# Kernel tuning notes

Measured on AMD Instinct MI355X. Metric: run time of the kernel, lower is better.

Reference implementation:

```python
import jax, jax.numpy as jnp
import numpy as np

TEMPERATURE = 0.07
EPS = 1e-8  # torch F.cosine_similarity eps


def reference(features):
    B, F, D = features.shape
    x = features.reshape(B * F, D)  # [N, D]
    # cosine similarity = normalized-dot; torch clamps norm at eps
    norm = jnp.maximum(jnp.linalg.norm(x, axis=-1, keepdims=True), EPS)
    xn = x / norm
    logits = (xn @ xn.T) / TEMPERATURE  # [N, N]
    # cross_entropy with labels = arange(N): mean(logsumexp - diagonal)
    lse = jax.scipy.special.logsumexp(logits, axis=-1)
    diag = jnp.diagonal(logits)
    return jnp.mean(lse - diag)


def setup_inputs() -> dict:
    key = jax.random.key(0)
    features = jax.random.normal(key, (512, 16, 512), dtype=jnp.float32)
    return {"features": features}
```

## Files before the change

### kernel.cpp

```cpp
#include <hip/hip_runtime.h>
#include <hip/hip_bf16.h>
#include <cstdint>

#define N_TOT 8192
#define DDIM  512
#define NBLK  64
#define NTRI  (NBLK * (NBLK + 1) / 2)
constexpr float INV_T = 1.0f / 0.07f;

typedef unsigned short u16;
typedef __attribute__((ext_vector_type(8))) short bf16x8_t;
typedef __attribute__((ext_vector_type(4))) float f32x4_t;


__device__ __forceinline__ u16 f2bf(float f) {
  uint32_t u = __float_as_uint(f);
  uint32_t r = (u + 0x7FFFu + ((u >> 16) & 1u)) >> 16;
  return (u16)r;
}

__device__ __forceinline__ void load16_to_lds(const void* g, void* l) {
  __builtin_amdgcn_global_load_lds(
      (const __attribute__((address_space(1))) unsigned int*)g,
      (__attribute__((address_space(3))) unsigned int*)l, 16, 0, 0);
}

__global__ __launch_bounds__(256) void normalize_kernel(const float* __restrict__ X,
                                                        u16* __restrict__ Xn,
                                                        float* __restrict__ tsum,
                                                        float* __restrict__ out) {
  if (blockIdx.x < 32) tsum[blockIdx.x * 256 + threadIdx.x] = 0.0f;
  if (blockIdx.x == 32 && threadIdx.x == 0) out[0] = 0.0f;
  const int lane = threadIdx.x & 63;
  const int row  = blockIdx.x * 4 + (threadIdx.x >> 6);
  const float4* xr = (const float4*)(X + (size_t)row * DDIM);
  float4 v0 = xr[lane];
  float4 v1 = xr[lane + 64];
  float s = v0.x * v0.x + v0.y * v0.y + v0.z * v0.z + v0.w * v0.w
          + v1.x * v1.x + v1.y * v1.y + v1.z * v1.z + v1.w * v1.w;
#pragma unroll
  for (int m = 1; m < 64; m <<= 1) s += __shfl_xor(s, m);
  const float scale = 1.0f / fmaxf(sqrtf(s), 1e-8f);
  ushort4 o0, o1;
  o0.x = f2bf(v0.x * scale); o0.y = f2bf(v0.y * scale);
  o0.z = f2bf(v0.z * scale); o0.w = f2bf(v0.w * scale);
  o1.x = f2bf(v1.x * scale); o1.y = f2bf(v1.y * scale);
  o1.z = f2bf(v1.z * scale); o1.w = f2bf(v1.w * scale);
  ushort4* orow = (ushort4*)(Xn + (size_t)row * DDIM);
  orow[lane]      = o0;
  orow[lane + 64] = o1;
}

__global__ __launch_bounds__(256, 4) void gemm_exp_rowsum(const u16* __restrict__ Xn,
                                                          float* __restrict__ tsum) {
  __shared__ __align__(16) u16 sA[128 * 64];
  __shared__ __align__(16) u16 sB[128 * 64];

  const int k = blockIdx.x;
  int bi = (int)((sqrtf(8.0f * (float)k + 1.0f) - 1.0f) * 0.5f);
  while ((bi + 1) * (bi + 2) / 2 <= k) ++bi;
  while (bi * (bi + 1) / 2 > k) --bi;
  const int bj = k - bi * (bi + 1) / 2;
  const int rowBase = bi * 128;
  const int colBase = bj * 128;
  const bool isDiag = (bi == bj);

  const int t    = threadIdx.x;
  const int lane = t & 63;
  const int l15  = lane & 15;
  const int quad = lane >> 4;
  const int w    = t >> 6;
  const int wm   = w >> 1;
  const int wn   = w & 1;

  f32x4_t acc[4][4];
#pragma unroll
  for (int i = 0; i < 4; i++)
#pragma unroll
    for (int j = 0; j < 4; j++) acc[i][j] = {0.f, 0.f, 0.f, 0.f};

  const int srow = t >> 3;
  const int jlog = ((t & 7) ^ (srow & 7)) * 8;
  const u16* gA = Xn + (size_t)(rowBase + srow) * DDIM + jlog;
  const u16* gB = Xn + (size_t)(colBase + srow) * DDIM + jlog;
  u16* lA = sA + t * 8;
  u16* lB = sB + t * 8;

  for (int k0 = 0; k0 < DDIM; k0 += 64) {
#pragma unroll
    for (int r = 0; r < 4; r++) {
      load16_to_lds(gA + (size_t)(r * 32) * DDIM + k0, lA + r * 256 * 8);
      load16_to_lds(gB + (size_t)(r * 32) * DDIM + k0, lB + r * 256 * 8);
    }
    __syncthreads();

#pragma unroll
    for (int kk = 0; kk < 2; kk++) {
      bf16x8_t a[4], b[4];
#pragma unroll
      for (int mi = 0; mi < 4; mi++) {
        const int row = wm * 64 + mi * 16 + l15;
        const int jp = (kk * 4 + quad) ^ (row & 7);
        a[mi] = *(const bf16x8_t*)&sA[row * 64 + jp * 8];
      }
#pragma unroll
      for (int ni = 0; ni < 4; ni++) {
        const int row = wn * 64 + ni * 16 + l15;
        const int jp = (kk * 4 + quad) ^ (row & 7);
        b[ni] = *(const bf16x8_t*)&sB[row * 64 + jp * 8];
      }
#pragma unroll
      for (int mi = 0; mi < 4; mi++)
#pragma unroll
        for (int ni = 0; ni < 4; ni++)
          acc[mi][ni] =
              __builtin_amdgcn_mfma_f32_16x16x32_bf16(a[mi], b[ni], acc[mi][ni], 0, 0, 0);
    }
    __syncthreads();
  }

  if (isDiag) {
#pragma unroll
    for (int mi = 0; mi < 4; mi++) {
#pragma unroll
      for (int r = 0; r < 4; r++) {
        const int row = rowBase + wm * 64 + mi * 16 + quad * 4 + r;
        float rs = 0.0f;
#pragma unroll
        for (int ni = 0; ni < 4; ni++) {
          const int col = colBase + wn * 64 + ni * 16 + l15;
          const float e = __expf((acc[mi][ni][r] - 1.0f) * INV_T);
          rs += (row == col) ? 0.0f : e;
        }
        rs += __shfl_xor(rs, 1);
        rs += __shfl_xor(rs, 2);
        rs += __shfl_xor(rs, 4);
        rs += __shfl_xor(rs, 8);
        if (l15 == 0) atomicAdd(&tsum[row], rs);
      }
    }
  } else {
    float csum[4] = {0.f, 0.f, 0.f, 0.f};
#pragma unroll
    for (int mi = 0; mi < 4; mi++) {
#pragma unroll
      for (int r = 0; r < 4; r++) {
        const int row = rowBase + wm * 64 + mi * 16 + quad * 4 + r;
        float rs = 0.0f;
#pragma unroll
        for (int ni = 0; ni < 4; ni++) {
          const float e = __expf((acc[mi][ni][r] - 1.0f) * INV_T);
          rs += e;
          csum[ni] += e;
        }
        rs += __shfl_xor(rs, 1);
        rs += __shfl_xor(rs, 2);
        rs += __shfl_xor(rs, 4);
        rs += __shfl_xor(rs, 8);
        if (l15 == 0) atomicAdd(&tsum[row], rs);
      }
    }
#pragma unroll
    for (int ni = 0; ni < 4; ni++) {
      csum[ni] += __shfl_xor(csum[ni], 16);
      csum[ni] += __shfl_xor(csum[ni], 32);
      if (quad == 0) atomicAdd(&tsum[colBase + wn * 64 + ni * 16 + l15], csum[ni]);
    }
  }
}

__global__ __launch_bounds__(256) void finalize_kernel(const float* __restrict__ tsum,
                                                       float* __restrict__ out) {
  const int i = blockIdx.x * 256 + threadIdx.x;
  float s = log1pf(tsum[i]);
#pragma unroll
  for (int m = 1; m < 64; m <<= 1) s += __shfl_xor(s, m);
  __shared__ float ws[4];
  if ((threadIdx.x & 63) == 0) ws[threadIdx.x >> 6] = s;
  __syncthreads();
  if (threadIdx.x == 0)
    atomicAdd(out, (ws[0] + ws[1] + ws[2] + ws[3]) * (1.0f / N_TOT));
}

extern "C" void kernel_launch(void* const* d_in, const int* in_sizes, int n_in,
                              void* d_out, int out_size, void* d_ws, size_t ws_size,
                              hipStream_t stream) {
  const float* X = (const float*)d_in[0];
  float* out = (float*)d_out;

  float* tsum = (float*)d_ws;
  u16* Xn = (u16*)((char*)d_ws + 65536);

  normalize_kernel<<<N_TOT / 4, 256, 0, stream>>>(X, Xn, tsum, out);
  gemm_exp_rowsum<<<NTRI, 256, 0, stream>>>(Xn, tsum);
  finalize_kernel<<<N_TOT / 256, 256, 0, stream>>>(tsum, out);
}
```

Measured before the change: 133.5 us.

## Quantize normalized features to FP8 and use scaled FP8 MFMA for Gram matrix

The normalize kernel now writes the normalized rows as FP8 (e4m3) instead of bf16. The GEMM uses the 16x16x128 f8f6f4 scaled MFMA with unit scales over 128-byte K tiles, and the LDS layout and swizzle are adjusted to match. This halves operand bytes and raises MFMA throughput per instruction, aiming to cut the compute-bound Gram-matrix time. The cost is a large precision loss in logits divided by 0.07, which may push the loss past tolerance, and launch bounds drop to 3 waves.

```diff
diff --git a/kernel.cpp b/kernel.cpp
--- a/kernel.cpp
+++ b/kernel.cpp
@@ -4,20 +4,15 @@
 
 #define N_TOT 8192
 #define DDIM  512
+#define DBYTES 512
 #define NBLK  64
 #define NTRI  (NBLK * (NBLK + 1) / 2)
 constexpr float INV_T = 1.0f / 0.07f;
 
-typedef unsigned short u16;
-typedef __attribute__((ext_vector_type(8))) short bf16x8_t;
+typedef uint8_t u8;
+typedef __attribute__((ext_vector_type(8))) int i32x8_t;
 typedef __attribute__((ext_vector_type(4))) float f32x4_t;
 
-
-__device__ __forceinline__ u16 f2bf(float f) {
-  uint32_t u = __float_as_uint(f);
-  uint32_t r = (u + 0x7FFFu + ((u >> 16) & 1u)) >> 16;
-  return (u16)r;
-}
 
 __device__ __forceinline__ void load16_to_lds(const void* g, void* l) {
   __builtin_amdgcn_global_load_lds(
@@ -26,7 +21,7 @@
 }
 
 __global__ __launch_bounds__(256) void normalize_kernel(const float* __restrict__ X,
-                                                        u16* __restrict__ Xn,
+                                                        u8* __restrict__ Xn,
                                                         float* __restrict__ tsum,
                                                         float* __restrict__ out) {
   if (blockIdx.x < 32) tsum[blockIdx.x * 256 + threadIdx.x] = 0.0f;
@@ -41,20 +36,19 @@
 #pragma unroll
   for (int m = 1; m < 64; m <<= 1) s += __shfl_xor(s, m);
   const float scale = 1.0f / fmaxf(sqrtf(s), 1e-8f);
-  ushort4 o0, o1;
-  o0.x = f2bf(v0.x * scale); o0.y = f2bf(v0.y * scale);
-  o0.z = f2bf(v0.z * scale); o0.w = f2bf(v0.w * scale);
-  o1.x = f2bf(v1.x * scale); o1.y = f2bf(v1.y * scale);
-  o1.z = f2bf(v1.z * scale); o1.w = f2bf(v1.w * scale);
-  ushort4* orow = (ushort4*)(Xn + (size_t)row * DDIM);
-  orow[lane]      = o0;
-  orow[lane + 64] = o1;
+  int w0 = __builtin_amdgcn_cvt_pk_fp8_f32(v0.x * scale, v0.y * scale, 0, 0);
+  w0     = __builtin_amdgcn_cvt_pk_fp8_f32(v0.z * scale, v0.w * scale, w0, 1);
+  int w1 = __builtin_amdgcn_cvt_pk_fp8_f32(v1.x * scale, v1.y * scale, 0, 0);
+  w1     = __builtin_amdgcn_cvt_pk_fp8_f32(v1.z * scale, v1.w * scale, w1, 1);
+  uint32_t* orow = (uint32_t*)(Xn + (size_t)row * DBYTES);
+  orow[lane]      = (uint32_t)w0;
+  orow[lane + 64] = (uint32_t)w1;
 }
 
-__global__ __launch_bounds__(256, 4) void gemm_exp_rowsum(const u16* __restrict__ Xn,
+__global__ __launch_bounds__(256, 3) void gemm_exp_rowsum(const u8* __restrict__ Xn,
                                                           float* __restrict__ tsum) {
-  __shared__ __align__(16) u16 sA[128 * 64];
-  __shared__ __align__(16) u16 sB[128 * 64];
+  __shared__ __align__(16) u8 sA[128 * 128];
+  __shared__ __align__(16) u8 sB[128 * 128];
 
   const int k = blockIdx.x;
   int bi = (int)((sqrtf(8.0f * (float)k + 1.0f) - 1.0f) * 0.5f);
@@ -80,42 +74,46 @@
     for (int j = 0; j < 4; j++) acc[i][j] = {0.f, 0.f, 0.f, 0.f};
 
   const int srow = t >> 3;
-  const int jlog = ((t & 7) ^ (srow & 7)) * 8;
-  const u16* gA = Xn + (size_t)(rowBase + srow) * DDIM + jlog;
-  const u16* gB = Xn + (size_t)(colBase + srow) * DDIM + jlog;
-  u16* lA = sA + t * 8;
-  u16* lB = sB + t * 8;
+  const int goff = ((t & 7) ^ (srow & 7)) * 16;
+  const u8* gA = Xn + (size_t)(rowBase + srow) * DBYTES + goff;
+  const u8* gB = Xn + (size_t)(colBase + srow) * DBYTES + goff;
+  u8* lA = sA + t * 16;
+  u8* lB = sB + t * 16;
 
-  for (int k0 = 0; k0 < DDIM; k0 += 64) {
+  for (int k0 = 0; k0 < DBYTES; k0 += 128) {
 #pragma unroll
     for (int r = 0; r < 4; r++) {
-      load16_to_lds(gA + (size_t)(r * 32) * DDIM + k0, lA + r * 256 * 8);
-      load16_to_lds(gB + (size_t)(r * 32) * DDIM + k0, lB + r * 256 * 8);
+      load16_to_lds(gA + (size_t)(r * 32) * DBYTES + k0, lA + r * 4096);
+      load16_to_lds(gB + (size_t)(r * 32) * DBYTES + k0, lB + r * 4096);
     }
     __syncthreads();
 
+    i32x8_t a[4], b[4];
 #pragma unroll
-    for (int kk = 0; kk < 2; kk++) {
-      bf16x8_t a[4], b[4];
+    for (int mi = 0; mi < 4; mi++) {
+      const int row = wm * 64 + mi * 16 + l15;
+      const int s0 = ((quad * 2) ^ (row & 7)) * 16;
+      const int s1 = ((quad * 2 + 1) ^ (row & 7)) * 16;
+      int4 lo = *(const int4*)&sA[row * 128 + s0];
+      int4 hi = *(const int4*)&sA[row * 128 + s1];
+      a[mi] = (i32x8_t){lo.x, lo.y, lo.z, lo.w, hi.x, hi.y, hi.z, hi.w};
+    }
 #pragma unroll
-      for (int mi = 0; mi < 4; mi++) {
-        const int row = wm * 64 + mi * 16 + l15;
-        const int jp = (kk * 4 + quad) ^ (row & 7);
-        a[mi] = *(const bf16x8_t*)&sA[row * 64 + jp * 8];
-      }
+    for (int ni = 0; ni < 4; ni++) {
+      const int row = wn * 64 + ni * 16 + l15;
+      const int s0 = ((quad * 2) ^ (row & 7)) * 16;
+      const int s1 = ((quad * 2 + 1) ^ (row & 7)) * 16;
+      int4 lo = *(const int4*)&sB[row * 128 + s0];
+      int4 hi = *(const int4*)&sB[row * 128 + s1];
+      b[ni] = (i32x8_t){lo.x, lo.y, lo.z, lo.w, hi.x, hi.y, hi.z, hi.w};
+    }
+
 #pragma unroll
-      for (int ni = 0; ni < 4; ni++) {
-        const int row = wn * 64 + ni * 16 + l15;
-        const int jp = (kk * 4 + quad) ^ (row & 7);
-        b[ni] = *(const bf16x8_t*)&sB[row * 64 + jp * 8];
-      }
+    for (int mi = 0; mi < 4; mi++)
 #pragma unroll
-      for (int mi = 0; mi < 4; mi++)
-#pragma unroll
-        for (int ni = 0; ni < 4; ni++)
-          acc[mi][ni] =
-              __builtin_amdgcn_mfma_f32_16x16x32_bf16(a[mi], b[ni], acc[mi][ni], 0, 0, 0);
-    }
+      for (int ni = 0; ni < 4; ni++)
+        acc[mi][ni] = __builtin_amdgcn_mfma_scale_f32_16x16x128_f8f6f4(
+            a[mi], b[ni], acc[mi][ni], 0, 0, 0, 0x7F7F7F7Fu, 0, 0x7F7F7F7Fu);
     __syncthreads();
   }
 
@@ -189,7 +187,7 @@
   float* out = (float*)d_out;
 
   float* tsum = (float*)d_ws;
-  u16* Xn = (u16*)((char*)d_ws + 65536);
+  u8* Xn = (u8*)d_ws + 65536;
 
   normalize_kernel<<<N_TOT / 4, 256, 0, stream>>>(X, Xn, tsum, out);
   gemm_exp_rowsum<<<NTRI, 256, 0, stream>>>(Xn, tsum);
```

New measurement: 116.0 us. -13.1%, faster.
